# Optimization experiments

Hardware: AMD Instinct MI355X
Metric: run time of the kernel (lower is better)

The kernel has to match this reference:

```python
import jax, jax.numpy as jnp
import numpy as np

C_Z = 128
C_H = 128
EPS = 1e-5


def _layer_norm(x, g, b):
    mu = jnp.mean(x, axis=-1, keepdims=True)
    var = jnp.var(x, axis=-1, keepdims=True)
    return (x - mu) * jax.lax.rsqrt(var + EPS) * g + b


def setup_inputs() -> dict:
    key = jax.random.key(0)
    ks = jax.random.split(key, 8)
    B, N = 1, 512
    z = jax.random.normal(ks[0], (B, N, N, C_Z), dtype=jnp.float32)
    mask = jnp.ones((B, N, N), dtype=jnp.float32)
    s = 0.02
    return {
        "z": z,
        "mask": mask,
        "ln_in_g": jnp.ones((C_Z,), jnp.float32),
        "ln_in_b": jnp.zeros((C_Z,), jnp.float32),
        "w_ap": jax.random.normal(ks[1], (C_Z, C_H), jnp.float32) * s,
        "b_ap": jnp.zeros((C_H,), jnp.float32),
        "w_ag": jax.random.normal(ks[2], (C_Z, C_H), jnp.float32) * s,
        "b_ag": jnp.zeros((C_H,), jnp.float32),
        "w_bp": jax.random.normal(ks[3], (C_Z, C_H), jnp.float32) * s,
        "b_bp": jnp.zeros((C_H,), jnp.float32),
        "w_bg": jax.random.normal(ks[4], (C_Z, C_H), jnp.float32) * s,
        "b_bg": jnp.zeros((C_H,), jnp.float32),
        "w_g": jax.random.normal(ks[5], (C_Z, C_Z), jnp.float32) * s,
        "b_g": jnp.zeros((C_Z,), jnp.float32),
        "ln_out_g": jnp.ones((C_H,), jnp.float32),
        "ln_out_b": jnp.zeros((C_H,), jnp.float32),
        "w_z": jax.random.normal(ks[6], (C_H, C_Z), jnp.float32) * s,
        "b_z": jnp.zeros((C_Z,), jnp.float32),
    }


def reference(z, mask, ln_in_g, ln_in_b, w_ap, b_ap, w_ag, b_ag,
              w_bp, b_bp, w_bg, b_bg, w_g, b_g, ln_out_g, ln_out_b, w_z, b_z):
    m = mask[..., None]                                  # [B,N,N,1]
    zn = _layer_norm(z, ln_in_g, ln_in_b)                # [B,N,N,Cz]
    a = m * jax.nn.sigmoid(zn @ w_ag + b_ag) * (zn @ w_ap + b_ap)  # [B,N,N,H]
    b = m * jax.nn.sigmoid(zn @ w_bg + b_bg) * (zn @ w_bp + b_bp)  # [B,N,N,H]
    # outgoing triangle: x[i,k] = sum_j a[i,j] * b[k,j]  (per hidden channel)
    x = jnp.einsum("bijh,bkjh->bikh", a, b)
    x = _layer_norm(x, ln_out_g, ln_out_b) @ w_z + b_z   # [B,N,N,Cz]
    g = jax.nn.sigmoid(zn @ w_g + b_g)
    return x * g
```

## Files before the change

kernel.cpp:

```cpp
#include <hip/hip_runtime.h>
#include <stdint.h>

#define NPOS 262144
#define EPS_LN 1e-5f
#define ZSTRIDE 272

typedef _Float16 f16x8_t __attribute__((ext_vector_type(8)));
typedef float f32x4_t __attribute__((ext_vector_type(4)));

static __device__ __forceinline__ unsigned short f2h(float f) {
    union { _Float16 h; unsigned short u; } v;
    v.h = (_Float16)f;
    return v.u;
}
static __device__ __forceinline__ float h2f(unsigned short u) {
    union { unsigned short u; _Float16 h; } v;
    v.u = u;
    return (float)v.h;
}
static __device__ __forceinline__ float sigmoidf_(float x) {
    return 1.0f / (1.0f + expf(-x));
}

#define GLOAD_LDS16(gp, lp) __builtin_amdgcn_global_load_lds( \
    (const __attribute__((address_space(1))) void*)(gp), \
    (__attribute__((address_space(3))) void*)(lp), 16, 0, 0)

__global__ __launch_bounds__(256)
void k_prep6(const float* w0, const float* w1, const float* w2,
             const float* w3, const float* w4, const float* w5,
             const float* lnog, unsigned short* wt) {
    const float* srcs[6] = {w0, w1, w2, w3, w4, w5};
    const float* src = srcs[blockIdx.x];
    unsigned short* dst = wt + blockIdx.x * 16384;
    const bool fold = (blockIdx.x == 4);
    for (int rep = 0; rep < 64; ++rep) {
        int idx = rep * 256 + threadIdx.x;
        int h = idx >> 7, k = idx & 127;
        float v = src[k * 128 + h];
        if (fold) v *= lnog[k];
        dst[idx] = f2h(v);
    }
}

__global__ __launch_bounds__(128)
void k_const(const float* w_z, const float* lnog, const float* lnob,
             float* c1, float* c2) {
    int c = threadIdx.x;
    float s1 = 0.f, s2 = 0.f;
    for (int k = 0; k < 128; ++k) {
        float wv = w_z[k * 128 + c];
        s1 += lnog[k] * wv;
        s2 += lnob[k] * wv;
    }
    c1[c] = s1;
    c2[c] = s2;
}

__global__ __launch_bounds__(512, 2)
void k1c(const float* __restrict__ z, const float* __restrict__ mask,
         const float* __restrict__ lng, const float* __restrict__ lnb,
         const unsigned short* __restrict__ wt,
         const float* __restrict__ b_ap, const float* __restrict__ b_ag,
         const float* __restrict__ b_bp, const float* __restrict__ b_bg,
         unsigned short* __restrict__ a_t, unsigned short* __restrict__ b_t,
         unsigned short* __restrict__ zn_out)
{
    __shared__ char sZn[128 * ZSTRIDE];
    const int t = threadIdx.x;
    const int lane = t & 63;
    const int w = t >> 6;
    const int g = lane >> 4;
    const int l15 = lane & 15;
    const int h = w * 16 + l15;
    const int p0 = blockIdx.x * 128;

    f16x8_t wapf[4], wagf[4], wbpf[4], wbgf[4];
    #pragma unroll
    for (int kk = 0; kk < 4; ++kk) {
        int off = h * 128 + kk * 32 + g * 8;
        wapf[kk] = *(const f16x8_t*)(wt + 0 * 16384 + off);
        wagf[kk] = *(const f16x8_t*)(wt + 1 * 16384 + off);
        wbpf[kk] = *(const f16x8_t*)(wt + 2 * 16384 + off);
        wbgf[kk] = *(const f16x8_t*)(wt + 3 * 16384 + off);
    }
    const float bap = b_ap[h], bag = b_ag[h];
    const float bbp = b_bp[h], bbg = b_bg[h];

    {
        const float g0 = lng[2 * lane], g1 = lng[2 * lane + 1];
        const float e0 = lnb[2 * lane], e1 = lnb[2 * lane + 1];
        for (int i = 0; i < 16; ++i) {
            int r = w * 16 + i;
            const float* zp = z + (size_t)(p0 + r) * 128 + 2 * lane;
            float v0 = zp[0], v1 = zp[1];
            float s = v0 + v1, s2 = v0 * v0 + v1 * v1;
            #pragma unroll
            for (int off = 1; off < 64; off <<= 1) {
                s  += __shfl_xor(s, off);
                s2 += __shfl_xor(s2, off);
            }
            float mu = s * (1.0f / 128.0f);
            float var = s2 * (1.0f / 128.0f) - mu * mu;
            float rstd = rsqrtf(var + EPS_LN);
            unsigned short h0 = f2h((v0 - mu) * rstd * g0 + e0);
            unsigned short h1 = f2h((v1 - mu) * rstd * g1 + e1);
            unsigned pk = h0 | ((unsigned)h1 << 16);
            *(unsigned*)(sZn + r * ZSTRIDE + lane * 4) = pk;
            *(unsigned*)(zn_out + (size_t)(p0 + r) * 128 + 2 * lane) = pk;
        }
    }
    __syncthreads();

    f32x4_t zero = {0.f, 0.f, 0.f, 0.f};
    for (int rt = 0; rt < 8; ++rt) {
        f32x4_t accAP = zero, accAG = zero, accBP = zero, accBG = zero;
        #pragma unroll
        for (int kk = 0; kk < 4; ++kk) {
            f16x8_t ax = *(const f16x8_t*)(sZn + (rt * 16 + l15) * ZSTRIDE + kk * 64 + g * 16);
            accAP = __builtin_amdgcn_mfma_f32_16x16x32_f16(ax, wapf[kk], accAP, 0, 0, 0);
            accAG = __builtin_amdgcn_mfma_f32_16x16x32_f16(ax, wagf[kk], accAG, 0, 0, 0);
            accBP = __builtin_amdgcn_mfma_f32_16x16x32_f16(ax, wbpf[kk], accBP, 0, 0, 0);
            accBG = __builtin_amdgcn_mfma_f32_16x16x32_f16(ax, wbgf[kk], accBG, 0, 0, 0);
        }
        int pb = p0 + rt * 16 + g * 4;
        unsigned short pka[4], pkb[4];
        #pragma unroll
        for (int r = 0; r < 4; ++r) {
            float m = mask[pb + r];
            pka[r] = f2h(m * sigmoidf_(accAG[r] + bag) * (accAP[r] + bap));
            pkb[r] = f2h(m * sigmoidf_(accBG[r] + bbg) * (accBP[r] + bbp));
        }
        uint2 sta, stb;
        sta.x = pka[0] | ((unsigned)pka[1] << 16);
        sta.y = pka[2] | ((unsigned)pka[3] << 16);
        stb.x = pkb[0] | ((unsigned)pkb[1] << 16);
        stb.y = pkb[2] | ((unsigned)pkb[3] << 16);
        *(uint2*)(a_t + (size_t)h * NPOS + pb) = sta;
        *(uint2*)(b_t + (size_t)h * NPOS + pb) = stb;
    }
}

__global__ __launch_bounds__(256, 2)
void k2_tri(const unsigned short* __restrict__ a_t,
            const unsigned short* __restrict__ b_t,
            unsigned short* __restrict__ x_t) {
    __shared__ char sA[16384];
    __shared__ char sB[16384];
    const int t = threadIdx.x;
    const int lane = t & 63;
    const int w = t >> 6;
    const int wr = w >> 1, wc = w & 1;
    const int h = blockIdx.y;
    const int i0 = (blockIdx.x >> 2) * 128;
    const int k0 = (blockIdx.x & 3) * 128;
    const unsigned short* Abase = a_t + (size_t)h * NPOS;
    const unsigned short* Bbase = b_t + (size_t)h * NPOS;

    f32x4_t zero = {0.f, 0.f, 0.f, 0.f};
    f32x4_t acc[4][4];
    #pragma unroll
    for (int m = 0; m < 4; ++m)
        #pragma unroll
        for (int n = 0; n < 4; ++n) acc[m][n] = zero;

    for (int kt = 0; kt < 8; ++kt) {
        #pragma unroll
        for (int pass = 0; pass < 4; ++pass) {
            int ci = pass * 256 + t;
            int row = ci >> 3, ch = ci & 7;
            const unsigned short* gA = Abase + (size_t)(i0 + row) * 512 + kt * 64 + ch * 8;
            const unsigned short* gB = Bbase + (size_t)(k0 + row) * 512 + kt * 64 + ch * 8;
            GLOAD_LDS16(gA, sA + w * 1024 + pass * 4096);
            GLOAD_LDS16(gB, sB + w * 1024 + pass * 4096);
        }
        __syncthreads();
        #pragma unroll
        for (int ks = 0; ks < 2; ++ks) {
            f16x8_t af[4], bf[4];
            #pragma unroll
            for (int m = 0; m < 4; ++m) {
                int ar = wr * 64 + m * 16 + (lane & 15);
                af[m] = *(const f16x8_t*)(sA + ar * 128 + ks * 64 + (lane >> 4) * 16);
            }
            #pragma unroll
            for (int n = 0; n < 4; ++n) {
                int br = wc * 64 + n * 16 + (lane & 15);
                bf[n] = *(const f16x8_t*)(sB + br * 128 + ks * 64 + (lane >> 4) * 16);
            }
            #pragma unroll
            for (int m = 0; m < 4; ++m)
                #pragma unroll
                for (int n = 0; n < 4; ++n)
                    acc[m][n] = __builtin_amdgcn_mfma_f32_16x16x32_f16(af[m], bf[n], acc[m][n], 0, 0, 0);
        }
        __syncthreads();
    }
    #pragma unroll
    for (int m = 0; m < 4; ++m) {
        int i = i0 + wr * 64 + m * 16 + (lane >> 4) * 4;
        #pragma unroll
        for (int n = 0; n < 4; ++n) {
            int k = k0 + wc * 64 + n * 16 + (lane & 15);
            #pragma unroll
            for (int r = 0; r < 4; ++r) {
                x_t[(size_t)h * NPOS + (size_t)(i + r) * 512 + k] = f2h(acc[m][n][r]);
            }
        }
    }
}

__global__ __launch_bounds__(512, 2)
void k3c(const unsigned short* __restrict__ x_t,
         const unsigned short* __restrict__ zn,
         const unsigned short* __restrict__ wt,
         const float* __restrict__ c1, const float* __restrict__ c2,
         const float* __restrict__ b_z, const float* __restrict__ b_g,
         float* __restrict__ out)
{
    __shared__ char sX[128 * ZSTRIDE];
    __shared__ float smu[128];
    __shared__ float srstd[128];
    const int t = threadIdx.x, lane = t & 63, w = t >> 6;
    const int g = lane >> 4;
    const int c = w * 16 + (lane & 15);
    const int p0 = blockIdx.x * 128;

    f16x8_t wzf[4], wgf[4];
    #pragma unroll
    for (int kk = 0; kk < 4; ++kk) {
        int off = c * 128 + kk * 32 + g * 8;
        wzf[kk] = *(const f16x8_t*)(wt + 4 * 16384 + off);
        wgf[kk] = *(const f16x8_t*)(wt + 5 * 16384 + off);
    }
    const float bzv = b_z[c], bgv = b_g[c];
    const float C1c = c1[c], C2c = c2[c];

    {
        const int hp = lane;
        const int ps = w * 16;
        const unsigned short* x0 = x_t + (size_t)(2 * hp) * NPOS + p0 + ps;
        const unsigned short* x1 = x_t + (size_t)(2 * hp + 1) * NPOS + p0 + ps;
        uint4 a0 = *(const uint4*)(x0);
        uint4 a1 = *(const uint4*)(x0 + 8);
        uint4 b0 = *(const uint4*)(x1);
        uint4 b1 = *(const uint4*)(x1 + 8);
        unsigned aw[8] = {a0.x, a0.y, a0.z, a0.w, a1.x, a1.y, a1.z, a1.w};
        unsigned bw[8] = {b0.x, b0.y, b0.z, b0.w, b1.x, b1.y, b1.z, b1.w};
        #pragma unroll
        for (int e = 0; e < 8; ++e) {
            int p = ps + 2 * e;
            *(unsigned*)(sX + p * ZSTRIDE + hp * 4) =
                (aw[e] & 0xffffu) | ((bw[e] & 0xffffu) << 16);
            *(unsigned*)(sX + (p + 1) * ZSTRIDE + hp * 4) =
                (aw[e] >> 16) | ((bw[e] >> 16) << 16);
        }
    }
    __syncthreads();
    {
        int pos = t >> 2, q = t & 3;
        float s = 0.f, s2 = 0.f;
        #pragma unroll
        for (int e = 0; e < 8; ++e) {
            uint2 vv = *(const uint2*)(sX + pos * ZSTRIDE + (q * 32 + e * 4) * 2);
            float v0 = h2f((unsigned short)(vv.x & 0xffffu));
            float v1 = h2f((unsigned short)(vv.x >> 16));
            float v2 = h2f((unsigned short)(vv.y & 0xffffu));
            float v3 = h2f((unsigned short)(vv.y >> 16));
            s  += v0 + v1 + v2 + v3;
            s2 += v0 * v0 + v1 * v1 + v2 * v2 + v3 * v3;
        }
        s  += __shfl_xor(s, 1);  s  += __shfl_xor(s, 2);
        s2 += __shfl_xor(s2, 1); s2 += __shfl_xor(s2, 2);
        float mu = s * (1.0f / 128.0f);
        float var = s2 * (1.0f / 128.0f) - mu * mu;
        if (q == 0) {
            smu[pos] = mu;
            srstd[pos] = rsqrtf(var + EPS_LN);
        }
    }
    __syncthreads();
    f32x4_t zero = {0.f, 0.f, 0.f, 0.f};
    for (int rt = 0; rt < 8; ++rt) {
        f32x4_t accX = zero, accG = zero;
        #pragma unroll
        for (int kk = 0; kk < 4; ++kk) {
            int row = rt * 16 + (lane & 15);
            f16x8_t ax = *(const f16x8_t*)(sX + row * ZSTRIDE + kk * 64 + g * 16);
            f16x8_t az = *(const f16x8_t*)(zn + (size_t)(p0 + row) * 128 + kk * 32 + g * 8);
            accX = __builtin_amdgcn_mfma_f32_16x16x32_f16(ax, wzf[kk], accX, 0, 0, 0);
            accG = __builtin_amdgcn_mfma_f32_16x16x32_f16(az, wgf[kk], accG, 0, 0, 0);
        }
        int lr0 = rt * 16 + g * 4;
        #pragma unroll
        for (int r = 0; r < 4; ++r) {
            float mu = smu[lr0 + r];
            float rstd = srstd[lr0 + r];
            float oz = rstd * (accX[r] - mu * C1c) + C2c + bzv;
            out[(size_t)(p0 + lr0 + r) * 128 + c] = oz * sigmoidf_(accG[r] + bgv);
        }
    }
}

extern "C" void kernel_launch(void* const* d_in, const int* in_sizes, int n_in,
                              void* d_out, int out_size, void* d_ws, size_t ws_size,
                              hipStream_t stream) {
    const float* z        = (const float*)d_in[0];
    const float* mask     = (const float*)d_in[1];
    const float* ln_in_g  = (const float*)d_in[2];
    const float* ln_in_b  = (const float*)d_in[3];
    const float* w_ap     = (const float*)d_in[4];
    const float* b_ap     = (const float*)d_in[5];
    const float* w_ag     = (const float*)d_in[6];
    const float* b_ag     = (const float*)d_in[7];
    const float* w_bp     = (const float*)d_in[8];
    const float* b_bp     = (const float*)d_in[9];
    const float* w_bg     = (const float*)d_in[10];
    const float* b_bg     = (const float*)d_in[11];
    const float* w_g      = (const float*)d_in[12];
    const float* b_g      = (const float*)d_in[13];
    const float* ln_out_g = (const float*)d_in[14];
    const float* ln_out_b = (const float*)d_in[15];
    const float* w_z      = (const float*)d_in[16];
    const float* b_z      = (const float*)d_in[17];
    float* out = (float*)d_out;

    char* ws = (char*)d_ws;
    const size_t MB64 = (size_t)NPOS * 128 * 2;
    unsigned short* wt   = (unsigned short*)(ws);
    float*          c1   = (float*)(ws + 786432);
    float*          c2   = (float*)(ws + 786432 + 512);
    unsigned short* a_t  = (unsigned short*)(ws + (1 << 20));
    unsigned short* b_t  = (unsigned short*)(ws + (1 << 20) + MB64);
    unsigned short* x_t  = (unsigned short*)(ws + (1 << 20) + 2 * MB64);
    unsigned short* zn_p = (unsigned short*)(ws + (1 << 20) + 3 * MB64);

    k_prep6<<<6, 256, 0, stream>>>(w_ap, w_ag, w_bp, w_bg, w_z, w_g, ln_out_g, wt);
    k_const<<<1, 128, 0, stream>>>(w_z, ln_out_g, ln_out_b, c1, c2);
    k1c<<<2048, 512, 0, stream>>>(z, mask, ln_in_g, ln_in_b, wt,
                                  b_ap, b_ag, b_bp, b_bg,
                                  a_t, b_t, zn_p);
    k2_tri<<<dim3(16, 128), 256, 0, stream>>>(a_t, b_t, x_t);
    k3c<<<2048, 512, 0, stream>>>(x_t, zn_p, wt, c1, c2, b_z, b_g, out);
}
```

Measured before the change: 349.1 us.

## Fold input layernorm into projection weights and post-GEMM affine correction

```diff
diff --git a/kernel.cpp b/kernel.cpp
--- a/kernel.cpp
+++ b/kernel.cpp
@@ -29,44 +29,49 @@
 __global__ __launch_bounds__(256)
 void k_prep6(const float* w0, const float* w1, const float* w2,
              const float* w3, const float* w4, const float* w5,
-             const float* lnog, unsigned short* wt) {
+             const float* lng, const float* lnog, unsigned short* wt) {
     const float* srcs[6] = {w0, w1, w2, w3, w4, w5};
     const float* src = srcs[blockIdx.x];
+    const float* fold = (blockIdx.x == 4) ? lnog : lng;
     unsigned short* dst = wt + blockIdx.x * 16384;
-    const bool fold = (blockIdx.x == 4);
     for (int rep = 0; rep < 64; ++rep) {
         int idx = rep * 256 + threadIdx.x;
         int h = idx >> 7, k = idx & 127;
-        float v = src[k * 128 + h];
-        if (fold) v *= lnog[k];
-        dst[idx] = f2h(v);
+        dst[idx] = f2h(src[k * 128 + h] * fold[k]);
     }
 }
 
 __global__ __launch_bounds__(128)
-void k_const(const float* w_z, const float* lnog, const float* lnob,
-             float* c1, float* c2) {
+void k_const(const float* wap, const float* wag, const float* wbp,
+             const float* wbg, const float* wz, const float* wg,
+             const float* lng, const float* lnb,
+             const float* lnog, const float* lnob, float* cc) {
+    const float* Ws[6] = {wap, wag, wbp, wbg, wz, wg};
+    const float* W = Ws[blockIdx.x];
+    const float* gv = (blockIdx.x == 4) ? lnog : lng;
+    const float* bv = (blockIdx.x == 4) ? lnob : lnb;
     int c = threadIdx.x;
     float s1 = 0.f, s2 = 0.f;
     for (int k = 0; k < 128; ++k) {
-        float wv = w_z[k * 128 + c];
-        s1 += lnog[k] * wv;
-        s2 += lnob[k] * wv;
-    }
-    c1[c] = s1;
-    c2[c] = s2;
+        float wv = W[k * 128 + c];
+        s1 += gv[k] * wv;
+        s2 += bv[k] * wv;
+    }
+    cc[blockIdx.x * 256 + c] = s1;
+    cc[blockIdx.x * 256 + 128 + c] = s2;
 }
 
 __global__ __launch_bounds__(512, 2)
-void k1c(const float* __restrict__ z, const float* __restrict__ mask,
-         const float* __restrict__ lng, const float* __restrict__ lnb,
-         const unsigned short* __restrict__ wt,
+void k1e(const float* __restrict__ z, const float* __restrict__ mask,
+         const unsigned short* __restrict__ wt, const float* __restrict__ cc,
          const float* __restrict__ b_ap, const float* __restrict__ b_ag,
          const float* __restrict__ b_bp, const float* __restrict__ b_bg,
          unsigned short* __restrict__ a_t, unsigned short* __restrict__ b_t,
-         unsigned short* __restrict__ zn_out)
+         unsigned short* __restrict__ z16, unsigned* __restrict__ mustd)
 {
-    __shared__ char sZn[128 * ZSTRIDE];
+    __shared__ char sZ[128 * ZSTRIDE];
+    __shared__ float smu[128];
+    __shared__ float srstd[128];
     const int t = threadIdx.x;
     const int lane = t & 63;
     const int w = t >> 6;
@@ -74,6 +79,41 @@
     const int l15 = lane & 15;
     const int h = w * 16 + l15;
     const int p0 = blockIdx.x * 128;
+
+    {
+        const int pos = t >> 2, q = t & 3;
+        const float* zp = z + (size_t)(p0 + pos) * 128 + q * 32;
+        float s = 0.f, s2 = 0.f;
+        uint4 pk[2];
+        unsigned* pw = (unsigned*)pk;
+        #pragma unroll
+        for (int e = 0; e < 8; ++e) {
+            float4 v = *(const float4*)(zp + e * 4);
+            pw[e] = 0;
+            unsigned lo = f2h(v.x) | ((unsigned)f2h(v.y) << 16);
+            unsigned hi = f2h(v.z) | ((unsigned)f2h(v.w) << 16);
+            if (e & 1) {
+                ((uint2*)pk)[e >> 1].y = 0;
+            }
+            ((unsigned*)pk)[(e >> 1) * 2 + 0] = (e & 1) ? ((unsigned*)pk)[(e >> 1) * 2 + 0] : lo;
+            ((unsigned*)pk)[e] = 0;
+            s += v.x + v.y + v.z + v.w;
+            s2 += v.x * v.x + v.y * v.y + v.z * v.z + v.w * v.w;
+            uint2 st; st.x = lo; st.y = hi;
+            *(uint2*)(sZ + pos * ZSTRIDE + (q * 32 + e * 4) * 2) = st;
+            *(uint2*)(z16 + (size_t)(p0 + pos) * 128 + q * 32 + e * 4) = st;
+        }
+        s  += __shfl_xor(s, 1);  s  += __shfl_xor(s, 2);
+        s2 += __shfl_xor(s2, 1); s2 += __shfl_xor(s2, 2);
+        float mu = s * (1.0f / 128.0f);
+        float var = s2 * (1.0f / 128.0f) - mu * mu;
+        float rstd = rsqrtf(var + EPS_LN);
+        if (q == 0) {
+            smu[pos] = mu;
+            srstd[pos] = rstd;
+            mustd[p0 + pos] = f2h(mu) | ((unsigned)f2h(rstd) << 16);
+        }
+    }
 
     f16x8_t wapf[4], wagf[4], wbpf[4], wbgf[4];
     #pragma unroll
@@ -84,32 +124,12 @@
         wbpf[kk] = *(const f16x8_t*)(wt + 2 * 16384 + off);
         wbgf[kk] = *(const f16x8_t*)(wt + 3 * 16384 + off);
     }
+    const float C1ap = cc[0 * 256 + h], C2ap = cc[0 * 256 + 128 + h];
+    const float C1ag = cc[1 * 256 + h], C2ag = cc[1 * 256 + 128 + h];
+    const float C1bp = cc[2 * 256 + h], C2bp = cc[2 * 256 + 128 + h];
+    const float C1bg = cc[3 * 256 + h], C2bg = cc[3 * 256 + 128 + h];
     const float bap = b_ap[h], bag = b_ag[h];
     const float bbp = b_bp[h], bbg = b_bg[h];
-
-    {
-        const float g0 = lng[2 * lane], g1 = lng[2 * lane + 1];
-        const float e0 = lnb[2 * lane], e1 = lnb[2 * lane + 1];
-        for (int i = 0; i < 16; ++i) {
-            int r = w * 16 + i;
-            const float* zp = z + (size_t)(p0 + r) * 128 + 2 * lane;
-            float v0 = zp[0], v1 = zp[1];
-            float s = v0 + v1, s2 = v0 * v0 + v1 * v1;
-            #pragma unroll
-            for (int off = 1; off < 64; off <<= 1) {
-                s  += __shfl_xor(s, off);
-                s2 += __shfl_xor(s2, off);
-            }
-            float mu = s * (1.0f / 128.0f);
-            float var = s2 * (1.0f / 128.0f) - mu * mu;
-            float rstd = rsqrtf(var + EPS_LN);
-            unsigned short h0 = f2h((v0 - mu) * rstd * g0 + e0);
-            unsigned short h1 = f2h((v1 - mu) * rstd * g1 + e1);
-            unsigned pk = h0 | ((unsigned)h1 << 16);
-            *(unsigned*)(sZn + r * ZSTRIDE + lane * 4) = pk;
-            *(unsigned*)(zn_out + (size_t)(p0 + r) * 128 + 2 * lane) = pk;
-        }
-    }
     __syncthreads();
 
     f32x4_t zero = {0.f, 0.f, 0.f, 0.f};
@@ -117,7 +137,7 @@
         f32x4_t accAP = zero, accAG = zero, accBP = zero, accBG = zero;
         #pragma unroll
         for (int kk = 0; kk < 4; ++kk) {
-            f16x8_t ax = *(const f16x8_t*)(sZn + (rt * 16 + l15) * ZSTRIDE + kk * 64 + g * 16);
+            f16x8_t ax = *(const f16x8_t*)(sZ + (rt * 16 + l15) * ZSTRIDE + kk * 64 + g * 16);
             accAP = __builtin_amdgcn_mfma_f32_16x16x32_f16(ax, wapf[kk], accAP, 0, 0, 0);
             accAG = __builtin_amdgcn_mfma_f32_16x16x32_f16(ax, wagf[kk], accAG, 0, 0, 0);
             accBP = __builtin_amdgcn_mfma_f32_16x16x32_f16(ax, wbpf[kk], accBP, 0, 0, 0);
@@ -127,9 +147,15 @@
         unsigned short pka[4], pkb[4];
         #pragma unroll
         for (int r = 0; r < 4; ++r) {
+            float mu = smu[rt * 16 + g * 4 + r];
+            float rstd = srstd[rt * 16 + g * 4 + r];
+            float vAP = rstd * (accAP[r] - mu * C1ap) + C2ap + bap;
+            float vAG = rstd * (accAG[r] - mu * C1ag) + C2ag + bag;
+            float vBP = rstd * (accBP[r] - mu * C1bp) + C2bp + bbp;
+            float vBG = rstd * (accBG[r] - mu * C1bg) + C2bg + bbg;
             float m = mask[pb + r];
-            pka[r] = f2h(m * sigmoidf_(accAG[r] + bag) * (accAP[r] + bap));
-            pkb[r] = f2h(m * sigmoidf_(accBG[r] + bbg) * (accBP[r] + bbp));
+            pka[r] = f2h(m * sigmoidf_(vAG) * vAP);
+            pkb[r] = f2h(m * sigmoidf_(vBG) * vBP);
         }
         uint2 sta, stb;
         sta.x = pka[0] | ((unsigned)pka[1] << 16);
@@ -211,16 +237,16 @@
 }
 
 __global__ __launch_bounds__(512, 2)
-void k3c(const unsigned short* __restrict__ x_t,
-         const unsigned short* __restrict__ zn,
-         const unsigned short* __restrict__ wt,
-         const float* __restrict__ c1, const float* __restrict__ c2,
+void k3d(const unsigned short* __restrict__ x_t,
+         const unsigned short* __restrict__ z16,
+         const unsigned* __restrict__ mustd,
+         const unsigned short* __restrict__ wt, const float* __restrict__ cc,
          const float* __restrict__ b_z, const float* __restrict__ b_g,
          float* __restrict__ out)
 {
     __shared__ char sX[128 * ZSTRIDE];
-    __shared__ float smu[128];
-    __shared__ float srstd[128];
+    __shared__ float smuX[128], srstdX[128];
+    __shared__ float smuZ[128], srstdZ[128];
     const int t = threadIdx.x, lane = t & 63, w = t >> 6;
     const int g = lane >> 4;
     const int c = w * 16 + (lane & 15);
@@ -234,7 +260,14 @@
         wgf[kk] = *(const f16x8_t*)(wt + 5 * 16384 + off);
     }
     const float bzv = b_z[c], bgv = b_g[c];
-    const float C1c = c1[c], C2c = c2[c];
+    const float C1z = cc[4 * 256 + c], C2z = cc[4 * 256 + 128 + c];
+    const float C1g = cc[5 * 256 + c], C2g = cc[5 * 256 + 128 + c];
+
+    if (t < 128) {
+        unsigned v = mustd[p0 + t];
+        smuZ[t] = h2f((unsigned short)(v & 0xffffu));
+        srstdZ[t] = h2f((unsigned short)(v >> 16));
+    }
 
     {
         const int hp = lane;
@@ -275,8 +308,8 @@
         float mu = s * (1.0f / 128.0f);
         float var = s2 * (1.0f / 128.0f) - mu * mu;
         if (q == 0) {
-            smu[pos] = mu;
-            srstd[pos] = rsqrtf(var + EPS_LN);
+            smuX[pos] = mu;
+            srstdX[pos] = rsqrtf(var + EPS_LN);
         }
     }
     __syncthreads();
@@ -287,17 +320,17 @@
         for (int kk = 0; kk < 4; ++kk) {
             int row = rt * 16 + (lane & 15);
             f16x8_t ax = *(const f16x8_t*)(sX + row * ZSTRIDE + kk * 64 + g * 16);
-            f16x8_t az = *(const f16x8_t*)(zn + (size_t)(p0 + row) * 128 + kk * 32 + g * 8);
+            f16x8_t az = *(const f16x8_t*)(z16 + (size_t)(p0 + row) * 128 + kk * 32 + g * 8);
             accX = __builtin_amdgcn_mfma_f32_16x16x32_f16(ax, wzf[kk], accX, 0, 0, 0);
             accG = __builtin_amdgcn_mfma_f32_16x16x32_f16(az, wgf[kk], accG, 0, 0, 0);
         }
         int lr0 = rt * 16 + g * 4;
         #pragma unroll
         for (int r = 0; r < 4; ++r) {
-            float mu = smu[lr0 + r];
-            float rstd = srstd[lr0 + r];
-            float oz = rstd * (accX[r] - mu * C1c) + C2c + bzv;
-            out[(size_t)(p0 + lr0 + r) * 128 + c] = oz * sigmoidf_(accG[r] + bgv);
+            int lr = lr0 + r;
+            float oz = srstdX[lr] * (accX[r] - smuX[lr] * C1z) + C2z + bzv;
+            float lg = srstdZ[lr] * (accG[r] - smuZ[lr] * C1g) + C2g + bgv;
+            out[(size_t)(p0 + lr) * 128 + c] = oz * sigmoidf_(lg);
         }
     }
 }
@@ -328,18 +361,20 @@
     char* ws = (char*)d_ws;
     const size_t MB64 = (size_t)NPOS * 128 * 2;
     unsigned short* wt   = (unsigned short*)(ws);
-    float*          c1   = (float*)(ws + 786432);
-    float*          c2   = (float*)(ws + 786432 + 512);
-    unsigned short* a_t  = (unsigned short*)(ws + (1 << 20));
-    unsigned short* b_t  = (unsigned short*)(ws + (1 << 20) + MB64);
-    unsigned short* x_t  = (unsigned short*)(ws + (1 << 20) + 2 * MB64);
-    unsigned short* zn_p = (unsigned short*)(ws + (1 << 20) + 3 * MB64);
-
-    k_prep6<<<6, 256, 0, stream>>>(w_ap, w_ag, w_bp, w_bg, w_z, w_g, ln_out_g, wt);
-    k_const<<<1, 128, 0, stream>>>(w_z, ln_out_g, ln_out_b, c1, c2);
-    k1c<<<2048, 512, 0, stream>>>(z, mask, ln_in_g, ln_in_b, wt,
+    float*          cc   = (float*)(ws + 786432);
+    unsigned*      mustd = (unsigned*)(ws + (1 << 20));
+    unsigned short* a_t  = (unsigned short*)(ws + (2 << 20));
+    unsigned short* b_t  = (unsigned short*)(ws + (2 << 20) + MB64);
+    unsigned short* x_t  = (unsigned short*)(ws + (2 << 20) + 2 * MB64);
+    unsigned short* z16  = (unsigned short*)(ws + (2 << 20) + 3 * MB64);
+
+    k_prep6<<<6, 256, 0, stream>>>(w_ap, w_ag, w_bp, w_bg, w_z, w_g,
+                                   ln_in_g, ln_out_g, wt);
+    k_const<<<6, 128, 0, stream>>>(w_ap, w_ag, w_bp, w_bg, w_z, w_g,
+                                   ln_in_g, ln_in_b, ln_out_g, ln_out_b, cc);
+    k1e<<<2048, 512, 0, stream>>>(z, mask, wt, cc,
                                   b_ap, b_ag, b_bp, b_bg,
-                                  a_t, b_t, zn_p);
+                                  a_t, b_t, z16, mustd);
     k2_tri<<<dim3(16, 128), 256, 0, stream>>>(a_t, b_t, x_t);
-    k3c<<<2048, 512, 0, stream>>>(x_t, zn_p, wt, c1, c2, b_z, b_g, out);
-}
+    k3d<<<2048, 512, 0, stream>>>(x_t, z16, mustd, wt, cc, b_z, b_g, out);
+}
```

New measurement: 342.3 us. Within noise of the previous version (-1.9%).
